# Performance work log

Hardware: AMD Instinct MI355X
Metric: run time of the kernel (lower is better)

The kernel has to match this reference:

```python
import jax, jax.numpy as jnp
import numpy as np

N_NODES = 50000
N_EDGES = 800000
HIDDEN = 128
IN_DIM = 6
N_ACTIONS = 64
NUM_GRAPHS = 512


def setup_inputs() -> dict:
    key = jax.random.key(0)
    ks = jax.random.split(key, 9)
    x = jax.random.normal(ks[0], (N_NODES, IN_DIM), dtype=jnp.float32)
    edge_index = jax.random.randint(ks[1], (2, N_EDGES), 0, N_NODES, dtype=jnp.int64)
    batch_number = jnp.sort(jax.random.randint(ks[2], (N_NODES,), 0, NUM_GRAPHS, dtype=jnp.int64))
    s1 = 1.0 / np.sqrt(IN_DIM)
    s2 = 1.0 / np.sqrt(HIDDEN)
    w1 = jax.random.uniform(ks[3], (IN_DIM, HIDDEN), jnp.float32, -s1, s1)
    b1 = jnp.zeros((HIDDEN,), jnp.float32)
    wl = jax.random.uniform(ks[4], (HIDDEN, HIDDEN), jnp.float32, -s2, s2)
    bl = jax.random.uniform(ks[5], (HIDDEN,), jnp.float32, -s2, s2)
    w2 = jax.random.uniform(ks[6], (HIDDEN, N_ACTIONS), jnp.float32, -s2, s2)
    b2 = jax.random.uniform(ks[7], (N_ACTIONS,), jnp.float32, -s2, s2)
    return {"x": x, "edge_index": edge_index, "batch_number": batch_number,
            "w1": w1, "b1": b1, "wl": wl, "bl": bl, "w2": w2, "b2": b2}


def _gcn_conv(x, edge_index, w, b):
    # PyG GCNConv: add self-loops, symmetric D^-1/2 (A+I) D^-1/2, linear first.
    n = x.shape[0]
    loop = jnp.arange(n, dtype=edge_index.dtype)
    src = jnp.concatenate([edge_index[0], loop])
    dst = jnp.concatenate([edge_index[1], loop])
    deg = jax.ops.segment_sum(jnp.ones_like(dst, dtype=x.dtype), dst, num_segments=n)
    dinv = jax.lax.rsqrt(jnp.maximum(deg, 1.0))  # deg >= 1 from self-loops
    norm = dinv[src] * dinv[dst]                  # [E+N]
    h = x @ w                                     # [N, hidden]
    msg = h[src] * norm[:, None]                  # gather + edge-wise scale
    return jax.ops.segment_sum(msg, dst, num_segments=n) + b


def reference(x, edge_index, batch_number, w1, b1, wl, bl, w2, b2):
    h = jax.nn.relu(_gcn_conv(x, edge_index, w1, b1))          # [N, hidden]
    # scatter_mean over graphs in the batch
    gsum = jax.ops.segment_sum(h, batch_number, num_segments=NUM_GRAPHS)
    cnt = jax.ops.segment_sum(jnp.ones((h.shape[0],), h.dtype), batch_number,
                              num_segments=NUM_GRAPHS)
    g = gsum / jnp.maximum(cnt, 1.0)[:, None]                  # [G, hidden]
    g = jax.nn.relu(g @ wl + bl)
    logits = g @ w2 + b2                                       # [G, actions]
    return jax.nn.log_softmax(logits, axis=1)
```

## Files before the change

kernel.cpp:

```cpp
#include <hip/hip_runtime.h>
#include <math.h>

#define N_NODES 50000
#define N_EDGES 800000
#define HID     128
#define N_ACT   64
#define N_GRAPH 512
#define N6      (N_NODES * 6)

#define NWF   2048
#define LOGW  11
#define WF    25
#define CAP   40960
#define CB    16
#define DC    16
#define EPB   2048
#define PB    ((N_EDGES + EPB - 1) / EPB)

#define NBLK    256
#define MAXSPAN 16

#define F_BUCKET 0
#define F_CURSOR (F_BUCKET + WF * CAP)
#define F_GSUM   (F_CURSOR + 32)
#define F_CNT    (F_GSUM + N_GRAPH * HID)
#define F_DINV   (F_CNT + N_GRAPH)
#define F_XSPAD  (F_DINV + N_NODES)
#define F_DEGP   (F_XSPAD + N_NODES * 8)
#define F_SPART  (F_DEGP + DC * N_NODES)
#define F_TOTAL  (F_SPART + CB * N6)
#define NEED_BYTES ((size_t)F_TOTAL * 4)
#define ZFLOATS (N_GRAPH * HID + N_GRAPH)


__global__ __launch_bounds__(512) void k_place(const int* __restrict__ ei,
                                               int* __restrict__ bucket,
                                               int* __restrict__ cursor,
                                               float* __restrict__ zbase) {
    __shared__ int lc[WF], lb[WF];
    int t = threadIdx.x;
    int tid = blockIdx.x * 512 + t;
    if (tid < ZFLOATS / 4) ((float4*)zbase)[tid] = make_float4(0, 0, 0, 0);

    if (t < WF) lc[t] = 0;
    __syncthreads();
    int e0 = blockIdx.x * EPB;
    int pk[4], wli[4];
#pragma unroll
    for (int i = 0; i < 4; ++i) {
        int e = e0 + i * 512 + t;
        wli[i] = -1;
        if (e < N_EDGES) {
            int src = ei[e], dst = ei[N_EDGES + e];
            int w = dst >> LOGW;
            int lp = atomicAdd(&lc[w], 1);
            pk[i] = ((dst - (w << LOGW)) << 16) | src;
            wli[i] = (w << 16) | lp;
        }
    }
    __syncthreads();
    if (t < WF) lb[t] = atomicAdd(&cursor[t], lc[t]);
    __syncthreads();
#pragma unroll
    for (int i = 0; i < 4; ++i) {
        if (wli[i] >= 0) {
            int w = wli[i] >> 16, lp = wli[i] & 0xffff;
            int pos = lb[w] + lp;
            if ((unsigned)pos < CAP) bucket[w * CAP + pos] = pk[i];
        }
    }
}

__global__ __launch_bounds__(512) void k_degp(const int* __restrict__ bucket,
                                              const int* __restrict__ cursor,
                                              float* __restrict__ degp) {
    __shared__ float hist[NWF];
    int w = blockIdx.x, c = blockIdx.y;
    int t = threadIdx.x;
    for (int i = t; i < NWF; i += 512) hist[i] = 0.0f;
    __syncthreads();
    int cw = min(cursor[w], CAP);
    const int* bp = bucket + w * CAP;
    const int stride = DC * 512;
    int e = c * 512 + t;
    for (; e + 3 * stride < cw; e += 4 * stride) {
        int p0 = bp[e], p1 = bp[e + stride], p2 = bp[e + 2 * stride], p3 = bp[e + 3 * stride];
        atomicAdd(&hist[((unsigned)p0) >> 16], 1.0f);
        atomicAdd(&hist[((unsigned)p1) >> 16], 1.0f);
        atomicAdd(&hist[((unsigned)p2) >> 16], 1.0f);
        atomicAdd(&hist[((unsigned)p3) >> 16], 1.0f);
    }
    for (; e < cw; e += stride) atomicAdd(&hist[((unsigned)bp[e]) >> 16], 1.0f);
    __syncthreads();
    int nb = w * NWF;
    int lim = min(NWF, N_NODES - nb);
    for (int i = t; i < lim; i += 512) degp[c * N_NODES + nb + i] = hist[i];
}

__global__ __launch_bounds__(256) void k_scale2(const float* __restrict__ degp,
                                                const float* __restrict__ x,
                                                float* __restrict__ dinv,
                                                float* __restrict__ xs_pad) {
    int n = blockIdx.x * 512 + 2 * threadIdx.x;
    if (n >= N_NODES) return;
    float d0 = 1.0f, d1 = 1.0f;
#pragma unroll
    for (int c = 0; c < DC; ++c) {
        d0 += degp[c * N_NODES + n];
        d1 += degp[c * N_NODES + n + 1];
    }
    float dv0 = rsqrtf(d0), dv1 = rsqrtf(d1);
    dinv[n] = dv0; dinv[n + 1] = dv1;
    const float4* xp = (const float4*)(x + (size_t)n * 6);
    float4 xa = xp[0], xb = xp[1], xc = xp[2];
    float4* op = (float4*)(xs_pad + (size_t)n * 8);
    op[0] = make_float4(xa.x * dv0, xa.y * dv0, xa.z * dv0, xa.w * dv0);
    op[1] = make_float4(xb.x * dv0, xb.y * dv0, 0.0f, 0.0f);
    op[2] = make_float4(xb.z * dv1, xb.w * dv1, xc.x * dv1, xc.y * dv1);
    op[3] = make_float4(xc.z * dv1, xc.w * dv1, 0.0f, 0.0f);
}

__global__ __launch_bounds__(512) void k_feat(const int* __restrict__ bucket,
                                              const int* __restrict__ cursor,
                                              const float* __restrict__ xs_pad,
                                              float* __restrict__ s_part) {
    __shared__ float h[NWF * 6];
    int w = blockIdx.x, c = blockIdx.y;
    int t = threadIdx.x;
    float4* h4 = (float4*)h;
    for (int i = t; i < NWF * 6 / 4; i += 512) h4[i] = make_float4(0, 0, 0, 0);
    __syncthreads();
    int cw = min(cursor[w], CAP);
    const int* bp = bucket + w * CAP;
    const int stride = CB * 512;
    int e = c * 512 + t;
    for (; e + 3 * stride < cw; e += 4 * stride) {
        int p0 = bp[e], p1 = bp[e + stride], p2 = bp[e + 2 * stride], p3 = bp[e + 3 * stride];
        const float4* q0 = (const float4*)(xs_pad + (size_t)(p0 & 0xffff) * 8);
        const float4* q1 = (const float4*)(xs_pad + (size_t)(p1 & 0xffff) * 8);
        const float4* q2 = (const float4*)(xs_pad + (size_t)(p2 & 0xffff) * 8);
        const float4* q3 = (const float4*)(xs_pad + (size_t)(p3 & 0xffff) * 8);
        float4 a0 = q0[0], b0 = q0[1];
        float4 a1 = q1[0], b1 = q1[1];
        float4 a2 = q2[0], b2 = q2[1];
        float4 a3 = q3[0], b3 = q3[1];
        float* hp;
        hp = &h[(((unsigned)p0) >> 16) * 6];
        atomicAdd(hp + 0, a0.x); atomicAdd(hp + 1, a0.y); atomicAdd(hp + 2, a0.z);
        atomicAdd(hp + 3, a0.w); atomicAdd(hp + 4, b0.x); atomicAdd(hp + 5, b0.y);
        hp = &h[(((unsigned)p1) >> 16) * 6];
        atomicAdd(hp + 0, a1.x); atomicAdd(hp + 1, a1.y); atomicAdd(hp + 2, a1.z);
        atomicAdd(hp + 3, a1.w); atomicAdd(hp + 4, b1.x); atomicAdd(hp + 5, b1.y);
        hp = &h[(((unsigned)p2) >> 16) * 6];
        atomicAdd(hp + 0, a2.x); atomicAdd(hp + 1, a2.y); atomicAdd(hp + 2, a2.z);
        atomicAdd(hp + 3, a2.w); atomicAdd(hp + 4, b2.x); atomicAdd(hp + 5, b2.y);
        hp = &h[(((unsigned)p3) >> 16) * 6];
        atomicAdd(hp + 0, a3.x); atomicAdd(hp + 1, a3.y); atomicAdd(hp + 2, a3.z);
        atomicAdd(hp + 3, a3.w); atomicAdd(hp + 4, b3.x); atomicAdd(hp + 5, b3.y);
    }
    for (; e < cw; e += stride) {
        int p = bp[e];
        const float4* q = (const float4*)(xs_pad + (size_t)(p & 0xffff) * 8);
        float4 a = q[0], b = q[1];
        float* hp = &h[(((unsigned)p) >> 16) * 6];
        atomicAdd(hp + 0, a.x); atomicAdd(hp + 1, a.y); atomicAdd(hp + 2, a.z);
        atomicAdd(hp + 3, a.w); atomicAdd(hp + 4, b.x); atomicAdd(hp + 5, b.y);
    }
    __syncthreads();
    int gb = w * NWF * 6;
    int lim = min(NWF * 6, N6 - gb);
    float4* sp4 = (float4*)(s_part + (size_t)c * N6 + gb);
    for (int i = t; i < lim / 4; i += 512) sp4[i] = h4[i];
}

__global__ __launch_bounds__(256) void k_node_f(const float* __restrict__ s_part,
                                                const float* __restrict__ xs_pad,
                                                const float* __restrict__ dinv,
                                                const int* __restrict__ batch,
                                                const float* __restrict__ w1,
                                                const float* __restrict__ b1,
                                                float* __restrict__ gsum,
                                                float* __restrict__ cnt) {
    __shared__ float sb[NBLK * 6];
    __shared__ float dvb[NBLK];
    __shared__ int   btb[NBLK];
    __shared__ float gacc[MAXSPAN][HID];
    __shared__ float gcnt[MAXSPAN];
    __shared__ int   sbnd[2];

    int nb0 = blockIdx.x * NBLK;
    int nEnd = min(nb0 + NBLK, N_NODES);
    int nCnt = nEnd - nb0;
    int lim = nCnt * 6;

    {
        float4* sb4 = (float4*)sb;
        int nv = lim >> 2;
        int g4base = (nb0 * 6) >> 2;
        for (int i = threadIdx.x; i < nv; i += 256) {
            float4 v = make_float4(0, 0, 0, 0);
#pragma unroll
            for (int c = 0; c < CB; ++c) {
                float4 p = ((const float4*)(s_part + (size_t)c * N6))[g4base + i];
                v.x += p.x; v.y += p.y; v.z += p.z; v.w += p.w;
            }
            sb4[i] = v;
        }
    }
    for (int i = threadIdx.x; i < nCnt; i += 256) {
        dvb[i] = dinv[nb0 + i];
        btb[i] = batch[nb0 + i];
    }
    if (threadIdx.x == 0) {
        sbnd[0] = (nb0 > 0) ? batch[nb0 - 1] : -1;
        sbnd[1] = (nEnd < N_NODES) ? batch[nEnd] : -1;
    }
    for (int i = threadIdx.x; i < MAXSPAN * HID; i += 256) ((float*)gacc)[i] = 0.0f;
    if (threadIdx.x < MAXSPAN) gcnt[threadIdx.x] = 0.0f;
    __syncthreads();

    for (int i = threadIdx.x; i < nCnt; i += 256) {
        const float4* xp = (const float4*)(xs_pad + (size_t)(nb0 + i) * 8);
        float4 a = xp[0], b = xp[1];
        float* sp = &sb[i * 6];
        sp[0] += a.x; sp[1] += a.y; sp[2] += a.z;
        sp[3] += a.w; sp[4] += b.x; sp[5] += b.y;
    }
    __syncthreads();

    int f = threadIdx.x & (HID - 1);
    int sub = threadIdx.x >> 7;
    float w1r[6];
#pragma unroll
    for (int k = 0; k < 6; ++k) w1r[k] = w1[k * HID + f];
    float b1f = b1[f];

    int bfirst = btb[0];
    int blast = btb[nCnt - 1];
    int span = blast - bfirst + 1;
    int bprev = sbnd[0], bnext = sbnd[1];
    int i0 = sub * (NBLK / 2);
    int i1 = min(i0 + (NBLK / 2), nCnt);

    if (span <= MAXSPAN) {
        float acc = 0.0f, rc = 0.0f;
        int curb = -1;
        for (int i = i0; i < i1; ++i) {
            const float* sp = &sb[i * 6];
            float t = 0.0f;
#pragma unroll
            for (int k = 0; k < 6; ++k) t = fmaf(sp[k], w1r[k], t);
            float a = fmaxf(fmaf(dvb[i], t, b1f), 0.0f);
            int b = btb[i];
            if (b != curb) {
                if (curb >= 0) {
                    atomicAdd(&gacc[curb - bfirst][f], acc);
                    if (f == 0) atomicAdd(&gcnt[curb - bfirst], rc);
                }
                acc = 0.0f; rc = 0.0f; curb = b;
            }
            acc += a; rc += 1.0f;
        }
        if (curb >= 0) {
            atomicAdd(&gacc[curb - bfirst][f], acc);
            if (f == 0) atomicAdd(&gcnt[curb - bfirst], rc);
        }
        __syncthreads();
        for (int idx = threadIdx.x; idx < span * HID; idx += 256) {
            int r = idx >> 7, ff = idx & (HID - 1);
            int gid = bfirst + r;
            float v = gacc[r][ff];
            if (gid == bprev || gid == bnext) atomicAdd(&gsum[gid * HID + ff], v);
            else gsum[gid * HID + ff] = v;
        }
        if (threadIdx.x < span) {
            int gid = bfirst + threadIdx.x;
            float v = gcnt[threadIdx.x];
            if (gid == bprev || gid == bnext) atomicAdd(&cnt[gid], v);
            else cnt[gid] = v;
        }
    } else {
        float acc = 0.0f, rc = 0.0f;
        int curb = -1;
        for (int i = i0; i < i1; ++i) {
            const float* sp = &sb[i * 6];
            float t = 0.0f;
#pragma unroll
            for (int k = 0; k < 6; ++k) t = fmaf(sp[k], w1r[k], t);
            float a = fmaxf(fmaf(dvb[i], t, b1f), 0.0f);
            int b = btb[i];
            if (b != curb) {
                if (curb >= 0) {
                    atomicAdd(&gsum[curb * HID + f], acc);
                    if (f == 0) atomicAdd(&cnt[curb], rc);
                }
                acc = 0.0f; rc = 0.0f; curb = b;
            }
            acc += a; rc += 1.0f;
        }
        if (curb >= 0) {
            atomicAdd(&gsum[curb * HID + f], acc);
            if (f == 0) atomicAdd(&cnt[curb], rc);
        }
    }
}

__global__ __launch_bounds__(512) void k_head4(const float* __restrict__ gsum,
                                               const float* __restrict__ cnt,
                                               const float* __restrict__ wl,
                                               const float* __restrict__ bl,
                                               const float* __restrict__ w2,
                                               const float* __restrict__ b2,
                                               float* __restrict__ out) {
    __shared__ float sg[4 * HID];
    __shared__ float sg2[4 * HID];
    int t = threadIdx.x;
    int sub = t >> 7, tt = t & (HID - 1);
    int g = blockIdx.x * 4 + sub;

    float ic = 1.0f / fmaxf(cnt[g], 1.0f);
    sg[sub * HID + tt] = gsum[g * HID + tt] * ic;
    __syncthreads();

    float acc = bl[tt];
    for (int k = 0; k < HID; ++k) acc = fmaf(sg[sub * HID + k], wl[k * HID + tt], acc);
    sg2[sub * HID + tt] = fmaxf(acc, 0.0f);
    __syncthreads();

    if (tt < N_ACT) {
        float l = b2[tt];
        for (int f = 0; f < HID; ++f) l = fmaf(sg2[sub * HID + f], w2[f * N_ACT + tt], l);
        float m = l;
#pragma unroll
        for (int off = 32; off > 0; off >>= 1) m = fmaxf(m, __shfl_xor(m, off));
        float e = expf(l - m);
        float ssum = e;
#pragma unroll
        for (int off = 32; off > 0; off >>= 1) ssum += __shfl_xor(ssum, off);
        out[g * N_ACT + tt] = l - m - logf(ssum);
    }
}


__global__ void k_init(float* __restrict__ deg, float* __restrict__ gsum,
                       float* __restrict__ cnt) {
    int i = blockIdx.x * blockDim.x + threadIdx.x;
    if (i < N_NODES) deg[i] = 1.0f;
    if (i < N_GRAPH * HID) gsum[i] = 0.0f;
    if (i < N_GRAPH) cnt[i] = 0.0f;
}

__global__ void k_deg(const int* __restrict__ ei, float* __restrict__ deg) {
    int e = blockIdx.x * blockDim.x + threadIdx.x;
    if (e < N_EDGES) atomicAdd(&deg[ei[N_EDGES + e]], 1.0f);
}

__global__ void k_scale(const float* __restrict__ x, const int* __restrict__ batch,
                        const float* __restrict__ deg, float* __restrict__ dinv,
                        float* __restrict__ xs, float* __restrict__ s,
                        float* __restrict__ cnt) {
    int n = blockIdx.x * blockDim.x + threadIdx.x;
    if (n >= N_NODES) return;
    float dv = rsqrtf(deg[n]);
    dinv[n] = dv;
#pragma unroll
    for (int k = 0; k < 6; ++k) {
        float v = x[n * 6 + k] * dv;
        xs[n * 6 + k] = v;
        s[n * 6 + k] = v;
    }
    atomicAdd(&cnt[batch[n]], 1.0f);
}

__global__ void k_scatter(const int* __restrict__ ei, const float* __restrict__ xs,
                          float* __restrict__ s) {
    int e = blockIdx.x * blockDim.x + threadIdx.x;
    if (e >= N_EDGES) return;
    int src = ei[e];
    int dst = ei[N_EDGES + e];
#pragma unroll
    for (int k = 0; k < 6; ++k)
        atomicAdd(&s[dst * 6 + k], xs[src * 6 + k]);
}

__global__ __launch_bounds__(256) void k_node(const float* __restrict__ s,
                                              const float* __restrict__ dinv,
                                              const int* __restrict__ batch,
                                              const float* __restrict__ w1,
                                              const float* __restrict__ b1,
                                              float* __restrict__ gsum) {
    int f = threadIdx.x & (HID - 1);
    int sub = threadIdx.x >> 7;
    int base = blockIdx.x * 16 + sub * 8;
    float w1r[6];
#pragma unroll
    for (int k = 0; k < 6; ++k) w1r[k] = w1[k * HID + f];
    float b1f = b1[f];
    float acc = 0.0f;
    int curb = -1;
    for (int i = 0; i < 8; ++i) {
        int n = base + i;
        if (n >= N_NODES) break;
        float t = 0.0f;
#pragma unroll
        for (int k = 0; k < 6; ++k) t = fmaf(s[n * 6 + k], w1r[k], t);
        float a = fmaxf(fmaf(dinv[n], t, b1f), 0.0f);
        int b = batch[n];
        if (b != curb) {
            if (curb >= 0) atomicAdd(&gsum[curb * HID + f], acc);
            acc = 0.0f;
            curb = b;
        }
        acc += a;
    }
    if (curb >= 0) atomicAdd(&gsum[curb * HID + f], acc);
}

__global__ __launch_bounds__(128) void k_head(const float* __restrict__ gsum,
                                              const float* __restrict__ cnt,
                                              const float* __restrict__ wl,
                                              const float* __restrict__ bl,
                                              const float* __restrict__ w2,
                                              const float* __restrict__ b2,
                                              float* __restrict__ out) {
    __shared__ float sg[HID];
    __shared__ float sg2[HID];
    int g = blockIdx.x;
    int t = threadIdx.x;

    float ic = 1.0f / fmaxf(cnt[g], 1.0f);
    sg[t] = gsum[g * HID + t] * ic;
    __syncthreads();

    float acc = bl[t];
    for (int k = 0; k < HID; ++k) acc = fmaf(sg[k], wl[k * HID + t], acc);
    sg2[t] = fmaxf(acc, 0.0f);
    __syncthreads();

    if (t < N_ACT) {
        float l = b2[t];
        for (int f = 0; f < HID; ++f) l = fmaf(sg2[f], w2[f * N_ACT + t], l);
        float m = l;
#pragma unroll
        for (int off = 32; off > 0; off >>= 1) m = fmaxf(m, __shfl_xor(m, off));
        float e = expf(l - m);
        float ssum = e;
#pragma unroll
        for (int off = 32; off > 0; off >>= 1) ssum += __shfl_xor(ssum, off);
        out[g * N_ACT + t] = l - m - logf(ssum);
    }
}


extern "C" void kernel_launch(void* const* d_in, const int* in_sizes, int n_in,
                              void* d_out, int out_size, void* d_ws, size_t ws_size,
                              hipStream_t stream) {
    const float* x     = (const float*)d_in[0];
    const int*   ei    = (const int*)d_in[1];
    const int*   batch = (const int*)d_in[2];
    const float* w1    = (const float*)d_in[3];
    const float* b1    = (const float*)d_in[4];
    const float* wl    = (const float*)d_in[5];
    const float* bl    = (const float*)d_in[6];
    const float* w2    = (const float*)d_in[7];
    const float* b2    = (const float*)d_in[8];
    float* out = (float*)d_out;
    float* ws = (float*)d_ws;

    if (ws_size >= NEED_BYTES) {
        int*   bucket = (int*)(ws + F_BUCKET);
        int*   cursor = (int*)(ws + F_CURSOR);
        float* gsum   = ws + F_GSUM;
        float* cnt    = ws + F_CNT;
        float* dinv   = ws + F_DINV;
        float* xs_pad = ws + F_XSPAD;
        float* degp   = ws + F_DEGP;
        float* s_part = ws + F_SPART;

        hipMemsetAsync(cursor, 0, 32 * sizeof(int), stream);
        k_place<<<PB, 512, 0, stream>>>(ei, bucket, cursor, gsum);
        k_degp<<<dim3(WF, DC), 512, 0, stream>>>(bucket, cursor, degp);
        k_scale2<<<(N_NODES + 511) / 512, 256, 0, stream>>>(degp, x, dinv, xs_pad);
        k_feat<<<dim3(WF, CB), 512, 0, stream>>>(bucket, cursor, xs_pad, s_part);
        k_node_f<<<(N_NODES + NBLK - 1) / NBLK, 256, 0, stream>>>(s_part, xs_pad, dinv, batch, w1, b1, gsum, cnt);
        k_head4<<<N_GRAPH / 4, 512, 0, stream>>>(gsum, cnt, wl, bl, w2, b2, out);
    } else {
        float* deg  = ws;
        float* dinv = deg + N_NODES;
        float* xs   = dinv + N_NODES;
        float* s    = xs + N6;
        float* gsum = s + N6;
        float* cnt  = gsum + N_GRAPH * HID;

        k_init<<<(N_GRAPH * HID + 255) / 256, 256, 0, stream>>>(deg, gsum, cnt);
        k_deg<<<(N_EDGES + 255) / 256, 256, 0, stream>>>(ei, deg);
        k_scale<<<(N_NODES + 255) / 256, 256, 0, stream>>>(x, batch, deg, dinv, xs, s, cnt);
        k_scatter<<<(N_EDGES + 255) / 256, 256, 0, stream>>>(ei, xs, s);
        k_node<<<(N_NODES + 15) / 16, 256, 0, stream>>>(s, dinv, batch, w1, b1, gsum);
        k_head<<<N_GRAPH, 128, 0, stream>>>(gsum, cnt, wl, bl, w2, b2, out);
    }
}
```

Before: 97.74 us.

## Fuse node transform, graph mean pooling and MLP head via sorted-batch graph offsets

Computes per-graph start offsets from the sorted batch vector inside the scaling kernel, then replaces the node kernel and head kernel with one kernel where each block owns four whole graphs. Each block reduces its graphs' node activations directly in registers, with no global atomics and no gsum/cnt buffers, and runs the MLP and log-softmax in place. This removes a launch, the zeroing pass and the global atomic traffic. In exchange, only 128 blocks run the node pass, so parallelism drops and the load is uneven across graphs, and the code relies on the batch vector being sorted.

```diff
diff --git a/kernel.cpp b/kernel.cpp
--- a/kernel.cpp
+++ b/kernel.cpp
@@ -17,31 +17,24 @@
 #define EPB   2048
 #define PB    ((N_EDGES + EPB - 1) / EPB)
 
-#define NBLK    256
-#define MAXSPAN 16
+#define MAXN  768
 
 #define F_BUCKET 0
 #define F_CURSOR (F_BUCKET + WF * CAP)
-#define F_GSUM   (F_CURSOR + 32)
-#define F_CNT    (F_GSUM + N_GRAPH * HID)
-#define F_DINV   (F_CNT + N_GRAPH)
+#define F_GSTART (F_CURSOR + 32)
+#define F_DINV   (F_GSTART + 516)
 #define F_XSPAD  (F_DINV + N_NODES)
 #define F_DEGP   (F_XSPAD + N_NODES * 8)
 #define F_SPART  (F_DEGP + DC * N_NODES)
 #define F_TOTAL  (F_SPART + CB * N6)
 #define NEED_BYTES ((size_t)F_TOTAL * 4)
-#define ZFLOATS (N_GRAPH * HID + N_GRAPH)
 
 
 __global__ __launch_bounds__(512) void k_place(const int* __restrict__ ei,
                                                int* __restrict__ bucket,
-                                               int* __restrict__ cursor,
-                                               float* __restrict__ zbase) {
+                                               int* __restrict__ cursor) {
     __shared__ int lc[WF], lb[WF];
     int t = threadIdx.x;
-    int tid = blockIdx.x * 512 + t;
-    if (tid < ZFLOATS / 4) ((float4*)zbase)[tid] = make_float4(0, 0, 0, 0);
-
     if (t < WF) lc[t] = 0;
     __syncthreads();
     int e0 = blockIdx.x * EPB;
@@ -97,10 +90,26 @@
     for (int i = t; i < lim; i += 512) degp[c * N_NODES + nb + i] = hist[i];
 }
 
+__device__ __forceinline__ void mark_gstart(const int* __restrict__ batch, int m,
+                                            int* __restrict__ gstart) {
+    int bm = batch[m];
+    if (m == 0) {
+        for (int g = 0; g <= bm; ++g) gstart[g] = 0;
+    } else {
+        int bp = batch[m - 1];
+        for (int g = bp + 1; g <= bm; ++g) gstart[g] = m;
+    }
+    if (m == N_NODES - 1) {
+        for (int g = bm + 1; g <= N_GRAPH; ++g) gstart[g] = N_NODES;
+    }
+}
+
 __global__ __launch_bounds__(256) void k_scale2(const float* __restrict__ degp,
                                                 const float* __restrict__ x,
+                                                const int* __restrict__ batch,
                                                 float* __restrict__ dinv,
-                                                float* __restrict__ xs_pad) {
+                                                float* __restrict__ xs_pad,
+                                                int* __restrict__ gstart) {
     int n = blockIdx.x * 512 + 2 * threadIdx.x;
     if (n >= N_NODES) return;
     float d0 = 1.0f, d1 = 1.0f;
@@ -118,6 +127,8 @@
     op[1] = make_float4(xb.x * dv0, xb.y * dv0, 0.0f, 0.0f);
     op[2] = make_float4(xb.z * dv1, xb.w * dv1, xc.x * dv1, xc.y * dv1);
     op[3] = make_float4(xc.z * dv1, xc.w * dv1, 0.0f, 0.0f);
+    mark_gstart(batch, n, gstart);
+    mark_gstart(batch, n + 1, gstart);
 }
 
 __global__ __launch_bounds__(512) void k_feat(const int* __restrict__ bucket,
@@ -173,163 +184,86 @@
     for (int i = t; i < lim / 4; i += 512) sp4[i] = h4[i];
 }
 
-__global__ __launch_bounds__(256) void k_node_f(const float* __restrict__ s_part,
-                                                const float* __restrict__ xs_pad,
-                                                const float* __restrict__ dinv,
-                                                const int* __restrict__ batch,
-                                                const float* __restrict__ w1,
-                                                const float* __restrict__ b1,
-                                                float* __restrict__ gsum,
-                                                float* __restrict__ cnt) {
-    __shared__ float sb[NBLK * 6];
-    __shared__ float dvb[NBLK];
-    __shared__ int   btb[NBLK];
-    __shared__ float gacc[MAXSPAN][HID];
-    __shared__ float gcnt[MAXSPAN];
-    __shared__ int   sbnd[2];
-
-    int nb0 = blockIdx.x * NBLK;
-    int nEnd = min(nb0 + NBLK, N_NODES);
-    int nCnt = nEnd - nb0;
-    int lim = nCnt * 6;
-
-    {
-        float4* sb4 = (float4*)sb;
-        int nv = lim >> 2;
-        int g4base = (nb0 * 6) >> 2;
-        for (int i = threadIdx.x; i < nv; i += 256) {
-            float4 v = make_float4(0, 0, 0, 0);
-#pragma unroll
-            for (int c = 0; c < CB; ++c) {
-                float4 p = ((const float4*)(s_part + (size_t)c * N6))[g4base + i];
-                v.x += p.x; v.y += p.y; v.z += p.z; v.w += p.w;
-            }
-            sb4[i] = v;
-        }
-    }
-    for (int i = threadIdx.x; i < nCnt; i += 256) {
-        dvb[i] = dinv[nb0 + i];
-        btb[i] = batch[nb0 + i];
-    }
-    if (threadIdx.x == 0) {
-        sbnd[0] = (nb0 > 0) ? batch[nb0 - 1] : -1;
-        sbnd[1] = (nEnd < N_NODES) ? batch[nEnd] : -1;
-    }
-    for (int i = threadIdx.x; i < MAXSPAN * HID; i += 256) ((float*)gacc)[i] = 0.0f;
-    if (threadIdx.x < MAXSPAN) gcnt[threadIdx.x] = 0.0f;
-    __syncthreads();
-
-    for (int i = threadIdx.x; i < nCnt; i += 256) {
-        const float4* xp = (const float4*)(xs_pad + (size_t)(nb0 + i) * 8);
-        float4 a = xp[0], b = xp[1];
-        float* sp = &sb[i * 6];
-        sp[0] += a.x; sp[1] += a.y; sp[2] += a.z;
-        sp[3] += a.w; sp[4] += b.x; sp[5] += b.y;
-    }
-    __syncthreads();
-
-    int f = threadIdx.x & (HID - 1);
-    int sub = threadIdx.x >> 7;
+__global__ __launch_bounds__(512) void k_nodehead(const float* __restrict__ s_part,
+                                                  const float* __restrict__ xs_pad,
+                                                  const float* __restrict__ dinv,
+                                                  const int* __restrict__ gstart,
+                                                  const float* __restrict__ w1,
+                                                  const float* __restrict__ b1,
+                                                  const float* __restrict__ wl,
+                                                  const float* __restrict__ bl,
+                                                  const float* __restrict__ w2,
+                                                  const float* __restrict__ b2,
+                                                  float* __restrict__ out) {
+    __shared__ float sb[MAXN * 6];
+    __shared__ float dvb[MAXN];
+    __shared__ float sg[4 * HID];
+    __shared__ float sg2[4 * HID];
+    __shared__ int gb[5];
+    int t = threadIdx.x;
+    int g0 = blockIdx.x * 4;
+    if (t < 5) gb[t] = gstart[g0 + t];
+    __syncthreads();
+    int ns = gb[0], ne = gb[4];
+    int sub = t >> 7, f = t & (HID - 1);
     float w1r[6];
 #pragma unroll
     for (int k = 0; k < 6; ++k) w1r[k] = w1[k * HID + f];
     float b1f = b1[f];
-
-    int bfirst = btb[0];
-    int blast = btb[nCnt - 1];
-    int span = blast - bfirst + 1;
-    int bprev = sbnd[0], bnext = sbnd[1];
-    int i0 = sub * (NBLK / 2);
-    int i1 = min(i0 + (NBLK / 2), nCnt);
-
-    if (span <= MAXSPAN) {
-        float acc = 0.0f, rc = 0.0f;
-        int curb = -1;
-        for (int i = i0; i < i1; ++i) {
+    float acc = 0.0f;
+
+    for (int base = ns; base < ne; base += MAXN) {
+        int cc = min(MAXN, ne - base);
+        __syncthreads();
+        {
+            float2* sb2 = (float2*)sb;
+            int nel = cc * 3;
+            int g2 = base * 3;
+            for (int i = t; i < nel; i += 512) {
+                float2 v = make_float2(0.0f, 0.0f);
+#pragma unroll
+                for (int c = 0; c < CB; ++c) {
+                    float2 p = ((const float2*)(s_part + (size_t)c * N6))[g2 + i];
+                    v.x += p.x; v.y += p.y;
+                }
+                sb2[i] = v;
+            }
+        }
+        for (int i = t; i < cc; i += 512) {
+            int n = base + i;
+            const float4* xp = (const float4*)(xs_pad + (size_t)n * 8);
+            float4 a = xp[0], bq = xp[1];
+            float* sp = &sb[i * 6];
+            sp[0] += a.x; sp[1] += a.y; sp[2] += a.z;
+            sp[3] += a.w; sp[4] += bq.x; sp[5] += bq.y;
+            dvb[i] = dinv[n];
+        }
+        __syncthreads();
+        int lo = max(gb[sub], base);
+        int hi = min(gb[sub + 1], base + cc);
+        for (int n = lo; n < hi; ++n) {
+            int i = n - base;
             const float* sp = &sb[i * 6];
-            float t = 0.0f;
-#pragma unroll
-            for (int k = 0; k < 6; ++k) t = fmaf(sp[k], w1r[k], t);
-            float a = fmaxf(fmaf(dvb[i], t, b1f), 0.0f);
-            int b = btb[i];
-            if (b != curb) {
-                if (curb >= 0) {
-                    atomicAdd(&gacc[curb - bfirst][f], acc);
-                    if (f == 0) atomicAdd(&gcnt[curb - bfirst], rc);
-                }
-                acc = 0.0f; rc = 0.0f; curb = b;
-            }
-            acc += a; rc += 1.0f;
-        }
-        if (curb >= 0) {
-            atomicAdd(&gacc[curb - bfirst][f], acc);
-            if (f == 0) atomicAdd(&gcnt[curb - bfirst], rc);
-        }
-        __syncthreads();
-        for (int idx = threadIdx.x; idx < span * HID; idx += 256) {
-            int r = idx >> 7, ff = idx & (HID - 1);
-            int gid = bfirst + r;
-            float v = gacc[r][ff];
-            if (gid == bprev || gid == bnext) atomicAdd(&gsum[gid * HID + ff], v);
-            else gsum[gid * HID + ff] = v;
-        }
-        if (threadIdx.x < span) {
-            int gid = bfirst + threadIdx.x;
-            float v = gcnt[threadIdx.x];
-            if (gid == bprev || gid == bnext) atomicAdd(&cnt[gid], v);
-            else cnt[gid] = v;
-        }
-    } else {
-        float acc = 0.0f, rc = 0.0f;
-        int curb = -1;
-        for (int i = i0; i < i1; ++i) {
-            const float* sp = &sb[i * 6];
-            float t = 0.0f;
-#pragma unroll
-            for (int k = 0; k < 6; ++k) t = fmaf(sp[k], w1r[k], t);
-            float a = fmaxf(fmaf(dvb[i], t, b1f), 0.0f);
-            int b = btb[i];
-            if (b != curb) {
-                if (curb >= 0) {
-                    atomicAdd(&gsum[curb * HID + f], acc);
-                    if (f == 0) atomicAdd(&cnt[curb], rc);
-                }
-                acc = 0.0f; rc = 0.0f; curb = b;
-            }
-            acc += a; rc += 1.0f;
-        }
-        if (curb >= 0) {
-            atomicAdd(&gsum[curb * HID + f], acc);
-            if (f == 0) atomicAdd(&cnt[curb], rc);
-        }
-    }
-}
-
-__global__ __launch_bounds__(512) void k_head4(const float* __restrict__ gsum,
-                                               const float* __restrict__ cnt,
-                                               const float* __restrict__ wl,
-                                               const float* __restrict__ bl,
-                                               const float* __restrict__ w2,
-                                               const float* __restrict__ b2,
-                                               float* __restrict__ out) {
-    __shared__ float sg[4 * HID];
-    __shared__ float sg2[4 * HID];
-    int t = threadIdx.x;
-    int sub = t >> 7, tt = t & (HID - 1);
-    int g = blockIdx.x * 4 + sub;
-
-    float ic = 1.0f / fmaxf(cnt[g], 1.0f);
-    sg[sub * HID + tt] = gsum[g * HID + tt] * ic;
-    __syncthreads();
-
-    float acc = bl[tt];
-    for (int k = 0; k < HID; ++k) acc = fmaf(sg[sub * HID + k], wl[k * HID + tt], acc);
-    sg2[sub * HID + tt] = fmaxf(acc, 0.0f);
-    __syncthreads();
-
-    if (tt < N_ACT) {
-        float l = b2[tt];
-        for (int f = 0; f < HID; ++f) l = fmaf(sg2[sub * HID + f], w2[f * N_ACT + tt], l);
+            float tv = 0.0f;
+#pragma unroll
+            for (int k = 0; k < 6; ++k) tv = fmaf(sp[k], w1r[k], tv);
+            acc += fmaxf(fmaf(dvb[i], tv, b1f), 0.0f);
+        }
+    }
+
+    int cnt = gb[sub + 1] - gb[sub];
+    float ic = 1.0f / fmaxf((float)cnt, 1.0f);
+    sg[sub * HID + f] = acc * ic;
+    __syncthreads();
+
+    float a2 = bl[f];
+    for (int k = 0; k < HID; ++k) a2 = fmaf(sg[sub * HID + k], wl[k * HID + f], a2);
+    sg2[sub * HID + f] = fmaxf(a2, 0.0f);
+    __syncthreads();
+
+    if (f < N_ACT) {
+        float l = b2[f];
+        for (int ff = 0; ff < HID; ++ff) l = fmaf(sg2[sub * HID + ff], w2[ff * N_ACT + f], l);
         float m = l;
 #pragma unroll
         for (int off = 32; off > 0; off >>= 1) m = fmaxf(m, __shfl_xor(m, off));
@@ -337,7 +271,7 @@
         float ssum = e;
 #pragma unroll
         for (int off = 32; off > 0; off >>= 1) ssum += __shfl_xor(ssum, off);
-        out[g * N_ACT + tt] = l - m - logf(ssum);
+        out[(g0 + sub) * N_ACT + f] = l - m - logf(ssum);
     }
 }
 
@@ -470,20 +404,19 @@
     if (ws_size >= NEED_BYTES) {
         int*   bucket = (int*)(ws + F_BUCKET);
         int*   cursor = (int*)(ws + F_CURSOR);
-        float* gsum   = ws + F_GSUM;
-        float* cnt    = ws + F_CNT;
+        int*   gstart = (int*)(ws + F_GSTART);
         float* dinv   = ws + F_DINV;
         float* xs_pad = ws + F_XSPAD;
         float* degp   = ws + F_DEGP;
         float* s_part = ws + F_SPART;
 
         hipMemsetAsync(cursor, 0, 32 * sizeof(int), stream);
-        k_place<<<PB, 512, 0, stream>>>(ei, bucket, cursor, gsum);
+        k_place<<<PB, 512, 0, stream>>>(ei, bucket, cursor);
         k_degp<<<dim3(WF, DC), 512, 0, stream>>>(bucket, cursor, degp);
-        k_scale2<<<(N_NODES + 511) / 512, 256, 0, stream>>>(degp, x, dinv, xs_pad);
+        k_scale2<<<(N_NODES + 511) / 512, 256, 0, stream>>>(degp, x, batch, dinv, xs_pad, gstart);
         k_feat<<<dim3(WF, CB), 512, 0, stream>>>(bucket, cursor, xs_pad, s_part);
-        k_node_f<<<(N_NODES + NBLK - 1) / NBLK, 256, 0, stream>>>(s_part, xs_pad, dinv, batch, w1, b1, gsum, cnt);
-        k_head4<<<N_GRAPH / 4, 512, 0, stream>>>(gsum, cnt, wl, bl, w2, b2, out);
+        k_nodehead<<<N_GRAPH / 4, 512, 0, stream>>>(s_part, xs_pad, dinv, gstart,
+                                                    w1, b1, wl, bl, w2, b2, out);
     } else {
         float* deg  = ws;
         float* dinv = deg + N_NODES;
```

Result: faster. 89.46 us (-8.5%).
